# Optimization experiments

Measured on AMD Instinct MI355X. Metric: run time of the kernel, lower is better.

Reference implementation:

```python
import jax, jax.numpy as jnp
import numpy as np

N_NODES = 8192
SEQ = 256
H = 32  # lstm_hdim == gcn_hdim


def lstm_layer(x, Wih, Whh, bih, bhh, return_seq):
    # x: [B, S, D] -> torch nn.LSTM, gate order i,f,g,o
    B = x.shape[0]
    Hd = Whh.shape[1]
    b = bih + bhh

    def step(carry, xt):
        h, c = carry
        z = xt @ Wih.T + h @ Whh.T + b  # [B, 4H]
        i, f, g, o = jnp.split(z, 4, axis=-1)
        c = jax.nn.sigmoid(f) * c + jax.nn.sigmoid(i) * jnp.tanh(g)
        h = jax.nn.sigmoid(o) * jnp.tanh(c)
        return (h, c), (h if return_seq else None)

    init = (jnp.zeros((B, Hd), x.dtype), jnp.zeros((B, Hd), x.dtype))
    (h_n, _), ys = jax.lax.scan(step, init, jnp.transpose(x, (1, 0, 2)))
    if return_seq:
        ys = jnp.transpose(ys, (1, 0, 2))  # [B, S, H]
    return ys, h_n


def layer_norm(x, g, b, eps=1e-5):
    mu = jnp.mean(x, axis=-1, keepdims=True)
    var = jnp.mean((x - mu) ** 2, axis=-1, keepdims=True)
    return (x - mu) * jax.lax.rsqrt(var + eps) * g + b


def gcn_conv(x, edge_index, edge_weight, W, bias, n_nodes):
    # PyG GCNConv with self-loops (fill 1.0) and symmetric normalization.
    h = x @ W  # transform first (in_dim -> out_dim)
    src, dst = edge_index[0], edge_index[1]
    deg = jax.ops.segment_sum(edge_weight, dst, num_segments=n_nodes) + 1.0  # +1 self loop
    dinv = jnp.where(deg > 0, jax.lax.rsqrt(deg), 0.0)
    norm = dinv[src] * edge_weight * dinv[dst]  # [E]
    agg = jax.ops.segment_sum(norm[:, None] * h[src], dst, num_segments=n_nodes)
    agg = agg + h * (dinv * dinv)[:, None]  # self-loop message
    return agg + bias


def setup_inputs() -> dict:
    key = jax.random.key(0)
    ks = jax.random.split(key, 20)
    s = 0.1
    d = {
        "x": jax.random.normal(ks[0], (N_NODES, SEQ), jnp.float32),
        "edge_weight": jax.random.uniform(ks[1], (262144,), jnp.float32),
        "Wih1": jax.random.normal(ks[2], (4 * H, 1)) * s,
        "Whh1": jax.random.normal(ks[3], (4 * H, H)) * s,
        "bih1": jax.random.normal(ks[4], (4 * H,)) * s,
        "bhh1": jax.random.normal(ks[5], (4 * H,)) * s,
        "ln1_g": jnp.ones((H,), jnp.float32),
        "ln1_b": jnp.zeros((H,), jnp.float32),
        "Wih2": jax.random.normal(ks[6], (4 * H, H)) * s,
        "Whh2": jax.random.normal(ks[7], (4 * H, H)) * s,
        "bih2": jax.random.normal(ks[8], (4 * H,)) * s,
        "bhh2": jax.random.normal(ks[9], (4 * H,)) * s,
        "Wg1": jax.random.normal(ks[10], (H, H)) * s,
        "bg1": jax.random.normal(ks[11], (H,)) * s,
        "Wg2": jax.random.normal(ks[12], (H, H)) * s,
        "bg2": jax.random.normal(ks[13], (H,)) * s,
        "Wfc": jax.random.normal(ks[14], (2, H + 1)) * s,
        "bfc": jax.random.normal(ks[15], (2,)) * s,
        "edge_index": jax.random.randint(ks[16], (2, 262144), 0, N_NODES, jnp.int64 if jax.config.jax_enable_x64 else jnp.int32),
    }
    return d


def reference(x, edge_weight, Wih1, Whh1, bih1, bhh1, ln1_g, ln1_b,
              Wih2, Whh2, bih2, bhh2, Wg1, bg1, Wg2, bg2, Wfc, bfc, edge_index):
    n = x.shape[0]
    xs = x[:, :, None]  # [B, S, 1]
    # Temporal module (batched over all samples; dropout off in eval).
    y1, _ = lstm_layer(xs, Wih1, Whh1, bih1, bhh1, return_seq=True)
    y1 = layer_norm(y1, ln1_g, ln1_b)
    _, h2 = lstm_layer(y1, Wih2, Whh2, bih2, bhh2, return_seq=False)  # [B, H]
    gcn_in = h2  # lstm_out.view(-1, lstm_hdim)
    # Spatial module: 2 GCNConv + ELU (dropout between layers is identity in eval).
    g = jax.nn.elu(gcn_conv(gcn_in, edge_index, edge_weight, Wg1, bg1, n))
    g = jax.nn.elu(gcn_conv(g, edge_index, edge_weight, Wg2, bg2, n))
    feat = jnp.concatenate([gcn_in, jnp.mean(g, axis=1, keepdims=True)], axis=1)  # [B, H+1]
    out = feat @ Wfc.T + bfc
    return jax.nn.log_softmax(out, axis=1)
```

## Files before the change

### kernel.cpp

```cpp
#include <hip/hip_runtime.h>

typedef __attribute__((ext_vector_type(8))) short short8;
typedef __attribute__((ext_vector_type(4))) float float4v;

#define NNODES 8192
#define SEQLEN 256
#define HSTR 40

static __device__ __forceinline__ unsigned short f2bf(float f) {
  union { float f; unsigned u; } v; v.f = f;
  unsigned r = v.u + 0x7FFFu + ((v.u >> 16) & 1u);
  return (unsigned short)(r >> 16);
}
static __device__ __forceinline__ void splitbf8(const float* v, short8& hi) {
#pragma unroll
  for (int j = 0; j < 8; ++j) hi[j] = (short)f2bf(v[j]);
}
static __device__ __forceinline__ float asf(unsigned u) {
  union { unsigned u; float f; } v; v.u = u; return v.f;
}

static __device__ __forceinline__ float lstm_cell(float zi, float zf, float zg,
                                                  float zo, float& c) {
  float ef = __builtin_amdgcn_exp2f(-zf);
  float ei = __builtin_amdgcn_exp2f(-zi);
  float eg = __builtin_amdgcn_exp2f(fminf(zg + zg, 60.f));
  float fterm = c * __builtin_amdgcn_rcpf(1.f + ef);
  float igt = (eg - 1.f) * __builtin_amdgcn_rcpf((1.f + ei) * (eg + 1.f));
  c = fterm + igt;
  float eo = __builtin_amdgcn_exp2f(-zo);
  float ec = __builtin_amdgcn_exp2f(fminf(2.88539008178f * c, 40.f));
  return (ec - 1.f) * __builtin_amdgcn_rcpf((1.f + eo) * (ec + 1.f));
}

static __device__ __forceinline__ void lstm_cell2(
    float z1i, float z1f, float z1g, float z1o,
    float z2i, float z2f, float z2g, float z2o,
    float& c1, float& c2, float& h1, float& h2) {
  float ef1 = __builtin_amdgcn_exp2f(-z1f);
  float ei1 = __builtin_amdgcn_exp2f(-z1i);
  float eg1 = __builtin_amdgcn_exp2f(fminf(z1g + z1g, 60.f));
  float A1 = 1.f + ef1;
  float D1 = (1.f + ei1) * (eg1 + 1.f);
  float R1 = __builtin_amdgcn_rcpf(A1 * D1);
  c1 = c1 * D1 * R1 + (eg1 - 1.f) * A1 * R1;

  float ef2 = __builtin_amdgcn_exp2f(-z2f);
  float ei2 = __builtin_amdgcn_exp2f(-z2i);
  float eg2 = __builtin_amdgcn_exp2f(fminf(z2g + z2g, 60.f));
  float A2 = 1.f + ef2;
  float D2 = (1.f + ei2) * (eg2 + 1.f);
  float R2 = __builtin_amdgcn_rcpf(A2 * D2);
  c2 = c2 * D2 * R2 + (eg2 - 1.f) * A2 * R2;

  float eo1 = __builtin_amdgcn_exp2f(-z1o);
  float ec1 = __builtin_amdgcn_exp2f(fminf(2.88539008178f * c1, 40.f));
  float eo2 = __builtin_amdgcn_exp2f(-z2o);
  float ec2 = __builtin_amdgcn_exp2f(fminf(2.88539008178f * c2, 40.f));
  float Q1 = (1.f + eo1) * (ec1 + 1.f);
  float Q2 = (1.f + eo2) * (ec2 + 1.f);
  float RQ = __builtin_amdgcn_rcpf(Q1 * Q2);
  h1 = (ec1 - 1.f) * Q2 * RQ;
  h2 = (ec2 - 1.f) * Q1 * RQ;
}

__global__ __launch_bounds__(512, 4)
void lstm_fused(const float* __restrict__ x,
                const float* __restrict__ Wih1, const float* __restrict__ Whh1,
                const float* __restrict__ bih1, const float* __restrict__ bhh1,
                const float* __restrict__ ln_g, const float* __restrict__ ln_b,
                const float* __restrict__ Wih2, const float* __restrict__ Whh2,
                const float* __restrict__ bih2, const float* __restrict__ bhh2,
                const float* __restrict__ Wg1,
                const int* __restrict__ ei, const float* __restrict__ ew,
                unsigned long long* __restrict__ pkc, int E,
                float* __restrict__ h2out, float* __restrict__ hWa)
{
  const int tid = threadIdx.x;
  const int w = tid >> 6;
  const int lane = tid & 63;
  const int c = lane & 15;
  const int q = lane >> 4;
  const int hid = w * 4 + q;
  const int nodeBase = blockIdx.x * 16;
  const float L = 1.44269504089f;

  __shared__ __align__(16) float xlds[16 * 260];
  __shared__ __align__(16) unsigned short h1p[2][16 * HSTR];
  __shared__ __align__(16) unsigned short h2p[2][16 * HSTR];
  __shared__ __align__(16) float wgbuf[32 * 33];
  __shared__ __align__(16) float h2f[16 * 33];

  for (int i = tid; i < 16 * 256; i += 512) {
    int nn = i >> 8, tt = i & 255;
    xlds[nn * 260 + tt] = x[(size_t)(nodeBase + nn) * SEQLEN + tt];
  }
  if (tid < 64) xlds[(tid >> 2) * 260 + 256 + (tid & 3)] = 0.f;
  for (int i = tid; i < 1024; i += 512) wgbuf[(i >> 5) * 33 + (i & 31)] = Wg1[i];

  for (int e = blockIdx.x * 512 + tid; e < E; e += gridDim.x * 512) {
    int d = ei[E + e];
    unsigned long long pay = (1ull << 40) |
        (unsigned long long)(unsigned)(ew[e] * 16777216.f + 0.5f);
    atomicAdd(&pkc[d], pay);
  }

  const int browF = (c & 3) * 32 + w * 4 + (c >> 2);
  short8 Bh1, Bi2, Bh2;
  {
    float v[8];
#pragma unroll
    for (int j = 0; j < 8; ++j) v[j] = L * Whh1[browF * 32 + q * 8 + j];
    splitbf8(v, Bh1);
#pragma unroll
    for (int j = 0; j < 8; ++j) v[j] = L * Wih2[browF * 32 + q * 8 + j] * ln_g[q * 8 + j];
    splitbf8(v, Bi2);
#pragma unroll
    for (int j = 0; j < 8; ++j) v[j] = L * Whh2[browF * 32 + q * 8 + j];
    splitbf8(v, Bh2);
  }
  const short8 Ones = {0x3F80, 0x3F80, 0x3F80, 0x3F80,
                       0x3F80, 0x3F80, 0x3F80, 0x3F80};

  float Gp[4], C1a[4], C2a[4];
#pragma unroll
  for (int r = 0; r < 4; ++r) {
    const int br = r * 32 + hid;
    float sG = 0.f, sB = 0.f;
    for (int k = 0; k < 32; ++k) {
      float wv = Wih2[br * 32 + k];
      sG += wv * ln_g[k];
      sB += wv * ln_b[k];
    }
    Gp[r] = L * sG;
    C1a[r] = L * (bih1[br] + bhh1[br]);
    C2a[r] = L * (sB + bih2[br] + bhh2[br]);
  }
  const float4v C1 = {C1a[0], C1a[1], C1a[2], C1a[3]};
  const float4v C2 = {C2a[0], C2a[1], C2a[2], C2a[3]};
  const float4v z4 = {0.f, 0.f, 0.f, 0.f};
  float w1v[4];
#pragma unroll
  for (int g = 0; g < 4; ++g) w1v[g] = L * Wih1[g * 32 + hid];

  const int hWr = c * HSTR + hid;
  const int hRd = c * HSTR + q * 8;

  short8 h1A = {0,0,0,0,0,0,0,0};
  short8 h2A = {0,0,0,0,0,0,0,0};
  float c1 = 0.f, c2 = 0.f, hv2 = 0.f;
  __syncthreads();

  {
    float xv = xlds[c * 260 + 0];
    float hv = lstm_cell(fmaf(xv, w1v[0], C1[0]), fmaf(xv, w1v[1], C1[1]),
                         fmaf(xv, w1v[2], C1[2]), fmaf(xv, w1v[3], C1[3]), c1);
    h1p[1][hWr] = f2bf(hv);
  }
  __syncthreads();
  h1A = *(const short8*)&h1p[1][hRd];

  auto step = [&](int t, int pl) {
    float xv = xlds[c * 260 + t + 1];
    float4v Cx = {fmaf(xv, w1v[0], C1[0]), fmaf(xv, w1v[1], C1[1]),
                  fmaf(xv, w1v[2], C1[2]), fmaf(xv, w1v[3], C1[3])};
    float4v za = __builtin_amdgcn_mfma_f32_16x16x32_bf16(Bh1, h1A, Cx, 0, 0, 0);
    float4v db = __builtin_amdgcn_mfma_f32_16x16x32_bf16(Bh2, h2A, C2, 0, 0, 0);
    float4v sv = __builtin_amdgcn_mfma_f32_16x16x32_bf16(Ones, h1A, z4, 0, 0, 0);

    float s2 = 0.f;
    {
      const unsigned* hw = (const unsigned*)&h1A;
#pragma unroll
      for (int j = 0; j < 4; ++j) {
        unsigned u = hw[j];
        float flo = asf(u << 16);
        float fhi = asf(u & 0xFFFF0000u);
        s2 = fmaf(flo, flo, s2);
        s2 = fmaf(fhi, fhi, s2);
      }
    }
    s2 += __shfl_xor(s2, 16, 64); s2 += __shfl_xor(s2, 32, 64);
    float mu = sv[0] * (1.f / 32.f);
    float var = fmaf(s2, 1.f / 32.f, -mu * mu);
    float rstd = __builtin_amdgcn_rsqf(var + 1e-5f);
    float mur = rstd * mu;

    float4v da = __builtin_amdgcn_mfma_f32_16x16x32_bf16(Bi2, h1A, z4, 0, 0, 0);

    float hv, hvb;
    lstm_cell2(za[0], za[1], za[2], za[3],
               fmaf(rstd, da[0], fmaf(-mur, Gp[0], db[0])),
               fmaf(rstd, da[1], fmaf(-mur, Gp[1], db[1])),
               fmaf(rstd, da[2], fmaf(-mur, Gp[2], db[2])),
               fmaf(rstd, da[3], fmaf(-mur, Gp[3], db[3])),
               c1, c2, hv, hvb);
    hv2 = hvb;

    unsigned pk;
    asm("v_cvt_pk_bf16_f32 %0, %1, %2" : "=v"(pk) : "v"(hv), "v"(hv2));
    h1p[pl][hWr] = (unsigned short)pk;
    h2p[pl][hWr] = (unsigned short)(pk >> 16);

    __syncthreads();
    h1A = *(const short8*)&h1p[pl][hRd];
    h2A = *(const short8*)&h2p[pl][hRd];
  };

  for (int t = 0; t < SEQLEN; t += 2) {
    step(t, 0);
    step(t + 1, 1);
  }

  h2out[(size_t)(nodeBase + c) * 32 + hid] = hv2;

  h2f[c * 33 + hid] = hv2;
  __syncthreads();
  {
    int nl = tid >> 5, j = tid & 31;
    float acc = 0.f;
#pragma unroll
    for (int k = 0; k < 32; ++k) acc = fmaf(h2f[nl * 33 + k], wgbuf[k * 33 + j], acc);
    hWa[(size_t)(nodeBase + nl) * 32 + j] = acc;
  }
}

__global__ __launch_bounds__(1024, 1)
void scan_k(const unsigned long long* __restrict__ pk, int* __restrict__ off,
            int* __restrict__ pos, float* __restrict__ dinv) {
  __shared__ int wtot[16];
  __shared__ int wexcl[16];
  int tid = threadIdx.x;
  int wv = tid >> 6, lane = tid & 63;
  int base = tid * 8;
  int v[8]; int sum = 0;
#pragma unroll
  for (int i = 0; i < 8; ++i) {
    unsigned long long u = pk[base + i];
    v[i] = (int)(u >> 40);
    float degv = (float)(u & 0xFFFFFFFFFFull) * (1.f / 16777216.f);
    dinv[base + i] = rsqrtf(degv + 1.0f);
    sum += v[i];
  }
  int incl = sum;
#pragma unroll
  for (int d = 1; d < 64; d <<= 1) {
    int t = __shfl_up(incl, d, 64);
    if (lane >= d) incl += t;
  }
  if (lane == 63) wtot[wv] = incl;
  __syncthreads();
  if (wv == 0 && lane < 16) {
    int wval = wtot[lane];
    int wincl = wval;
#pragma unroll
    for (int d = 1; d < 16; d <<= 1) {
      int t = __shfl_up(wincl, d, 64);
      if (lane >= d) wincl += t;
    }
    wexcl[lane] = wincl - wval;
  }
  __syncthreads();
  int run = wexcl[wv] + (incl - sum);
#pragma unroll
  for (int i = 0; i < 8; ++i) {
    off[base + i] = run; pos[base + i] = run; run += v[i];
  }
  if (tid == 1023) off[8192] = run;
}

__global__ void scatter_k(const int* __restrict__ ei, const float* __restrict__ ew,
                          const float* __restrict__ dinv, int* __restrict__ pos,
                          int2* __restrict__ ed, int E) {
  int e = blockIdx.x * 256 + threadIdx.x;
  if (e >= E) return;
  int sidx = ei[e], d = ei[E + e];
  int p = atomicAdd(&pos[d], 1);
  int2 pay;
  pay.x = sidx;
  pay.y = __float_as_int(dinv[sidx] * ew[e] * dinv[d]);
  ed[p] = pay;
}

__global__ __launch_bounds__(512, 4)
void gather_mid_k(const int* __restrict__ off, const int2* __restrict__ ed,
                  const float* __restrict__ dinv, const float* __restrict__ hWa,
                  const float* __restrict__ bg1, const float* __restrict__ Wg2,
                  float* __restrict__ aggB) {
  __shared__ float wg[32 * 33];
  __shared__ float g1buf[16][33];
  int tid = threadIdx.x;
  for (int i = tid; i < 1024; i += 512) wg[(i >> 5) * 33 + (i & 31)] = Wg2[i];
  int nl = tid >> 5, j = tid & 31;
  int node = blockIdx.x * 16 + nl;
  float dv = dinv[node];
  float a0 = dv * dv * hWa[(size_t)node * 32 + j];
  float a1 = 0.f, a2 = 0.f, a3 = 0.f;
  int p0 = off[node], p1 = off[node + 1];
  int p = p0;
  for (; p + 3 < p1; p += 4) {
    int2 e0 = ed[p], e1 = ed[p + 1], e2 = ed[p + 2], e3 = ed[p + 3];
    a0 = fmaf(__int_as_float(e0.y), hWa[(size_t)e0.x * 32 + j], a0);
    a1 = fmaf(__int_as_float(e1.y), hWa[(size_t)e1.x * 32 + j], a1);
    a2 = fmaf(__int_as_float(e2.y), hWa[(size_t)e2.x * 32 + j], a2);
    a3 = fmaf(__int_as_float(e3.y), hWa[(size_t)e3.x * 32 + j], a3);
  }
  for (; p < p1; ++p) {
    int2 e0 = ed[p];
    a0 = fmaf(__int_as_float(e0.y), hWa[(size_t)e0.x * 32 + j], a0);
  }
  float v = (a0 + a1) + (a2 + a3) + bg1[j];
  g1buf[nl][j] = (v > 0.f) ? v : expm1f(v);
  __syncthreads();
  float acc = 0.f;
#pragma unroll
  for (int k = 0; k < 32; ++k) acc = fmaf(g1buf[nl][k], wg[k * 33 + j], acc);
  aggB[(size_t)node * 32 + j] = acc;
}

__global__ __launch_bounds__(512, 4)
void gather_final_k(const int* __restrict__ off, const int2* __restrict__ ed,
                    const float* __restrict__ dinv, const float* __restrict__ aggB,
                    const float* __restrict__ bg2, const float* __restrict__ h2o,
                    const float* __restrict__ Wfc, const float* __restrict__ bfc,
                    float* __restrict__ out) {
  int tid = threadIdx.x;
  int nl = tid >> 5, j = tid & 31;
  int node = blockIdx.x * 16 + nl;
  float dv = dinv[node];
  float a0 = dv * dv * aggB[(size_t)node * 32 + j];
  float a1 = 0.f, a2 = 0.f, a3 = 0.f;
  int p0 = off[node], p1 = off[node + 1];
  int p = p0;
  for (; p + 3 < p1; p += 4) {
    int2 e0 = ed[p], e1 = ed[p + 1], e2 = ed[p + 2], e3 = ed[p + 3];
    a0 = fmaf(__int_as_float(e0.y), aggB[(size_t)e0.x * 32 + j], a0);
    a1 = fmaf(__int_as_float(e1.y), aggB[(size_t)e1.x * 32 + j], a1);
    a2 = fmaf(__int_as_float(e2.y), aggB[(size_t)e2.x * 32 + j], a2);
    a3 = fmaf(__int_as_float(e3.y), aggB[(size_t)e3.x * 32 + j], a3);
  }
  for (; p < p1; ++p) {
    int2 e0 = ed[p];
    a0 = fmaf(__int_as_float(e0.y), aggB[(size_t)e0.x * 32 + j], a0);
  }
  float v = (a0 + a1) + (a2 + a3) + bg2[j];
  float e = (v > 0.f) ? v : expm1f(v);
  float h2v = h2o[(size_t)node * 32 + j];
  float p0s = h2v * Wfc[j];
  float p1s = h2v * Wfc[33 + j];
#pragma unroll
  for (int m = 1; m < 32; m <<= 1) {
    e   += __shfl_xor(e, m, 32);
    p0s += __shfl_xor(p0s, m, 32);
    p1s += __shfl_xor(p1s, m, 32);
  }
  if (j == 0) {
    float mean = e * (1.f / 32.f);
    float o0 = p0s + mean * Wfc[32] + bfc[0];
    float o1 = p1s + mean * Wfc[65] + bfc[1];
    float mx = fmaxf(o0, o1);
    float l = mx + logf(expf(o0 - mx) + expf(o1 - mx));
    out[node * 2 + 0] = o0 - l;
    out[node * 2 + 1] = o1 - l;
  }
}

extern "C" void kernel_launch(void* const* d_in, const int* in_sizes, int n_in,
                              void* d_out, int out_size, void* d_ws, size_t ws_size,
                              hipStream_t stream) {
  const float* x    = (const float*)d_in[0];
  const float* ew   = (const float*)d_in[1];
  const float* Wih1 = (const float*)d_in[2];
  const float* Whh1 = (const float*)d_in[3];
  const float* bih1 = (const float*)d_in[4];
  const float* bhh1 = (const float*)d_in[5];
  const float* ln_g = (const float*)d_in[6];
  const float* ln_b = (const float*)d_in[7];
  const float* Wih2 = (const float*)d_in[8];
  const float* Whh2 = (const float*)d_in[9];
  const float* bih2 = (const float*)d_in[10];
  const float* bhh2 = (const float*)d_in[11];
  const float* Wg1  = (const float*)d_in[12];
  const float* bg1  = (const float*)d_in[13];
  const float* Wg2  = (const float*)d_in[14];
  const float* bg2  = (const float*)d_in[15];
  const float* Wfc  = (const float*)d_in[16];
  const float* bfc  = (const float*)d_in[17];
  const int* ei     = (const int*)d_in[18];
  float* out = (float*)d_out;
  const int E = in_sizes[1];

  float* ws   = (float*)d_ws;
  float* h2o  = ws;
  float* hWa  = ws + 262144;
  float* aggB = ws + 524288;
  unsigned long long* pk = (unsigned long long*)(ws + 786432);
  float* dinv = ws + 802816;
  int*   off  = (int*)(ws + 811008);
  int*   pos  = (int*)(ws + 819208);
  int2*  ed   = (int2*)(ws + 827400);

  hipMemsetAsync((void*)pk, 0, 8192 * sizeof(unsigned long long), stream);
  hipLaunchKernelGGL(lstm_fused, dim3(NNODES / 16), dim3(512), 0, stream,
                     x, Wih1, Whh1, bih1, bhh1, ln_g, ln_b,
                     Wih2, Whh2, bih2, bhh2, Wg1, ei, ew, pk, E, h2o, hWa);
  hipLaunchKernelGGL(scan_k, dim3(1), dim3(1024), 0, stream, pk, off, pos, dinv);
  hipLaunchKernelGGL(scatter_k, dim3((E + 255) / 256), dim3(256), 0, stream, ei, ew, dinv, pos, ed, E);
  hipLaunchKernelGGL(gather_mid_k, dim3(NNODES / 16), dim3(512), 0, stream,
                     off, ed, dinv, hWa, bg1, Wg2, aggB);
  hipLaunchKernelGGL(gather_final_k, dim3(NNODES / 16), dim3(512), 0, stream,
                     off, ed, dinv, aggB, bg2, h2o, Wfc, bfc, out);
}
```

Baseline: 355.9 us.

## Fuse degree scan and edge scatter into LSTM kernel via extra spin-wait blocks

Adds 128 extra blocks to the LSTM kernel. They wait on a global counter until every LSTM block has finished its degree atomics, then one block runs the prefix scan and the rest run the CSR edge scatter, all while the LSTM recurrence is still executing. This removes two kernel launches and hides the scan and scatter work behind the long LSTM loop. The cost is spin-waiting blocks holding CU slots, and the scheme relies on all LSTM blocks being co-resident or scheduled ahead of the waiters, otherwise it can deadlock.

```diff
diff --git a/kernel.cpp b/kernel.cpp
--- a/kernel.cpp
+++ b/kernel.cpp
@@ -74,23 +74,100 @@
                 const float* __restrict__ Wg1,
                 const int* __restrict__ ei, const float* __restrict__ ew,
                 unsigned long long* __restrict__ pkc, int E,
+                unsigned* __restrict__ ctr, unsigned* __restrict__ flag,
+                int* __restrict__ offp, int* __restrict__ posp,
+                float* __restrict__ dinvp, int2* __restrict__ edp,
                 float* __restrict__ h2out, float* __restrict__ hWa)
 {
   const int tid = threadIdx.x;
   const int w = tid >> 6;
   const int lane = tid & 63;
+
+  __shared__ __align__(16) float xlds[16 * 260];
+  __shared__ __align__(16) unsigned short h1p[2][16 * HSTR];
+  __shared__ __align__(16) unsigned short h2p[2][16 * HSTR];
+  __shared__ __align__(16) float wgbuf[32 * 33];
+  __shared__ __align__(16) float h2f[16 * 33];
+  __shared__ int scanw[16];
+
+  if (blockIdx.x >= NNODES / 16) {
+    const int eb = blockIdx.x - NNODES / 16;
+    if (tid == 0) {
+      while (__hip_atomic_load(ctr, __ATOMIC_ACQUIRE,
+                               __HIP_MEMORY_SCOPE_AGENT) < (unsigned)(NNODES / 16))
+        __builtin_amdgcn_s_sleep(16);
+    }
+    __syncthreads();
+    if (eb == 0) {
+      const int base2 = tid * 16;
+      int v[16]; int sum = 0;
+#pragma unroll
+      for (int i = 0; i < 16; ++i) {
+        unsigned long long u = __hip_atomic_load(&pkc[base2 + i], __ATOMIC_RELAXED,
+                                                 __HIP_MEMORY_SCOPE_AGENT);
+        v[i] = (int)(u >> 40);
+        float degv = (float)(u & 0xFFFFFFFFFFull) * (1.f / 16777216.f);
+        dinvp[base2 + i] = rsqrtf(degv + 1.0f);
+        sum += v[i];
+      }
+      int incl = sum;
+#pragma unroll
+      for (int d = 1; d < 64; d <<= 1) {
+        int t = __shfl_up(incl, d, 64);
+        if (lane >= d) incl += t;
+      }
+      if (lane == 63) scanw[w] = incl;
+      __syncthreads();
+      if (w == 0 && lane < 8) {
+        int wval = scanw[lane];
+        int wincl = wval;
+#pragma unroll
+        for (int d = 1; d < 8; d <<= 1) {
+          int t = __shfl_up(wincl, d, 64);
+          if (lane >= d) wincl += t;
+        }
+        scanw[8 + lane] = wincl - wval;
+      }
+      __syncthreads();
+      int run = scanw[8 + w] + (incl - sum);
+#pragma unroll
+      for (int i = 0; i < 16; ++i) {
+        offp[base2 + i] = run; posp[base2 + i] = run; run += v[i];
+      }
+      if (tid == 511) offp[8192] = run;
+      __syncthreads();
+      if (tid == 0)
+        __hip_atomic_store(flag, 1u, __ATOMIC_RELEASE, __HIP_MEMORY_SCOPE_AGENT);
+    } else {
+      if (tid == 0) {
+        while (__hip_atomic_load(flag, __ATOMIC_ACQUIRE,
+                                 __HIP_MEMORY_SCOPE_AGENT) == 0u)
+          __builtin_amdgcn_s_sleep(16);
+      }
+      __syncthreads();
+    }
+    const int base = eb * 512 + tid;
+#pragma unroll
+    for (int k = 0; k < 4; ++k) {
+      int e = base + k * 65536;
+      if (e < E) {
+        int sidx = ei[e], d = ei[E + e];
+        int p = atomicAdd(&posp[d], 1);
+        int2 pay;
+        pay.x = sidx;
+        pay.y = __float_as_int(dinvp[sidx] * ew[e] * dinvp[d]);
+        edp[p] = pay;
+      }
+    }
+    return;
+  }
+
   const int c = lane & 15;
   const int q = lane >> 4;
   const int hid = w * 4 + q;
   const int nodeBase = blockIdx.x * 16;
   const float L = 1.44269504089f;
 
-  __shared__ __align__(16) float xlds[16 * 260];
-  __shared__ __align__(16) unsigned short h1p[2][16 * HSTR];
-  __shared__ __align__(16) unsigned short h2p[2][16 * HSTR];
-  __shared__ __align__(16) float wgbuf[32 * 33];
-  __shared__ __align__(16) float h2f[16 * 33];
-
   for (int i = tid; i < 16 * 256; i += 512) {
     int nn = i >> 8, tt = i & 255;
     xlds[nn * 260 + tt] = x[(size_t)(nodeBase + nn) * SEQLEN + tt];
@@ -98,7 +175,7 @@
   if (tid < 64) xlds[(tid >> 2) * 260 + 256 + (tid & 3)] = 0.f;
   for (int i = tid; i < 1024; i += 512) wgbuf[(i >> 5) * 33 + (i & 31)] = Wg1[i];
 
-  for (int e = blockIdx.x * 512 + tid; e < E; e += gridDim.x * 512) {
+  for (int e = blockIdx.x * 512 + tid; e < E; e += (NNODES / 16) * 512) {
     int d = ei[E + e];
     unsigned long long pay = (1ull << 40) |
         (unsigned long long)(unsigned)(ew[e] * 16777216.f + 0.5f);
@@ -150,6 +227,8 @@
   short8 h2A = {0,0,0,0,0,0,0,0};
   float c1 = 0.f, c2 = 0.f, hv2 = 0.f;
   __syncthreads();
+  if (tid == 0)
+    __hip_atomic_fetch_add(ctr, 1u, __ATOMIC_RELEASE, __HIP_MEMORY_SCOPE_AGENT);
 
   {
     float xv = xlds[c * 260 + 0];
@@ -223,63 +302,6 @@
     for (int k = 0; k < 32; ++k) acc = fmaf(h2f[nl * 33 + k], wgbuf[k * 33 + j], acc);
     hWa[(size_t)(nodeBase + nl) * 32 + j] = acc;
   }
-}
-
-__global__ __launch_bounds__(1024, 1)
-void scan_k(const unsigned long long* __restrict__ pk, int* __restrict__ off,
-            int* __restrict__ pos, float* __restrict__ dinv) {
-  __shared__ int wtot[16];
-  __shared__ int wexcl[16];
-  int tid = threadIdx.x;
-  int wv = tid >> 6, lane = tid & 63;
-  int base = tid * 8;
-  int v[8]; int sum = 0;
-#pragma unroll
-  for (int i = 0; i < 8; ++i) {
-    unsigned long long u = pk[base + i];
-    v[i] = (int)(u >> 40);
-    float degv = (float)(u & 0xFFFFFFFFFFull) * (1.f / 16777216.f);
-    dinv[base + i] = rsqrtf(degv + 1.0f);
-    sum += v[i];
-  }
-  int incl = sum;
-#pragma unroll
-  for (int d = 1; d < 64; d <<= 1) {
-    int t = __shfl_up(incl, d, 64);
-    if (lane >= d) incl += t;
-  }
-  if (lane == 63) wtot[wv] = incl;
-  __syncthreads();
-  if (wv == 0 && lane < 16) {
-    int wval = wtot[lane];
-    int wincl = wval;
-#pragma unroll
-    for (int d = 1; d < 16; d <<= 1) {
-      int t = __shfl_up(wincl, d, 64);
-      if (lane >= d) wincl += t;
-    }
-    wexcl[lane] = wincl - wval;
-  }
-  __syncthreads();
-  int run = wexcl[wv] + (incl - sum);
-#pragma unroll
-  for (int i = 0; i < 8; ++i) {
-    off[base + i] = run; pos[base + i] = run; run += v[i];
-  }
-  if (tid == 1023) off[8192] = run;
-}
-
-__global__ void scatter_k(const int* __restrict__ ei, const float* __restrict__ ew,
-                          const float* __restrict__ dinv, int* __restrict__ pos,
-                          int2* __restrict__ ed, int E) {
-  int e = blockIdx.x * 256 + threadIdx.x;
-  if (e >= E) return;
-  int sidx = ei[e], d = ei[E + e];
-  int p = atomicAdd(&pos[d], 1);
-  int2 pay;
-  pay.x = sidx;
-  pay.y = __float_as_int(dinv[sidx] * ew[e] * dinv[d]);
-  ed[p] = pay;
 }
 
 __global__ __launch_bounds__(512, 4)
@@ -397,15 +419,17 @@
   unsigned long long* pk = (unsigned long long*)(ws + 786432);
   float* dinv = ws + 802816;
   int*   off  = (int*)(ws + 811008);
+  unsigned* ctr = (unsigned*)(ws + 819202);
+  unsigned* flag = ctr + 1;
   int*   pos  = (int*)(ws + 819208);
   int2*  ed   = (int2*)(ws + 827400);
 
   hipMemsetAsync((void*)pk, 0, 8192 * sizeof(unsigned long long), stream);
-  hipLaunchKernelGGL(lstm_fused, dim3(NNODES / 16), dim3(512), 0, stream,
+  hipMemsetAsync((void*)ctr, 0, 2 * sizeof(unsigned), stream);
+  hipLaunchKernelGGL(lstm_fused, dim3(NNODES / 16 + 128), dim3(512), 0, stream,
                      x, Wih1, Whh1, bih1, bhh1, ln_g, ln_b,
-                     Wih2, Whh2, bih2, bhh2, Wg1, ei, ew, pk, E, h2o, hWa);
-  hipLaunchKernelGGL(scan_k, dim3(1), dim3(1024), 0, stream, pk, off, pos, dinv);
-  hipLaunchKernelGGL(scatter_k, dim3((E + 255) / 256), dim3(256), 0, stream, ei, ew, dinv, pos, ed, E);
+                     Wih2, Whh2, bih2, bhh2, Wg1, ei, ew, pk, E,
+                     ctr, flag, off, pos, dinv, ed, h2o, hWa);
   hipLaunchKernelGGL(gather_mid_k, dim3(NNODES / 16), dim3(512), 0, stream,
                      off, ed, dinv, hWa, bg1, Wg2, aggB);
   hipLaunchKernelGGL(gather_final_k, dim3(NNODES / 16), dim3(512), 0, stream,
```

After: 375.8 us. +5.6%, slower.
